# Performance work log

Hardware: AMD Instinct MI355X
Metric: run time of the kernel (lower is better)

The kernel has to match this reference:

```python
import jax, jax.numpy as jnp
import numpy as np

GRID = 16
PAD = 32
RADIUS = 8
SIGMA = 1.5
B = 8192
N_SEEDS = 24


def setup_inputs() -> dict:
    key = jax.random.key(0)
    k1, k2 = jax.random.split(key)
    # predicted seeds: (x, y, phase), coords in [0, GRID)
    output = jax.random.uniform(k1, (B, N_SEEDS * 3), dtype=jnp.float32) * GRID
    # target seeds: (x, y, amp), coords in [0, 2*GRID)
    targets = jax.random.uniform(k2, (B, N_SEEDS * 3), dtype=jnp.float32) * (2 * GRID)
    return {"output": output, "targets": targets}


def _forward(output, targets):
    Bn = output.shape[0]
    seeds = output.reshape(Bn, -1, 3)   # (B, N, 3): x, y, phase
    tgt = targets.reshape(Bn, -1, 3)    # (B, M, 3): x, y, amp

    # --- discrete Voronoi on GRID x GRID (vectorized over batch) ---
    c = jnp.arange(GRID, dtype=output.dtype)
    xx, yy = jnp.meshgrid(c, c, indexing='ij')  # (GRID, GRID)
    dist = jnp.sqrt((xx[None, :, :, None] - seeds[:, None, None, :, 0]) ** 2
                    + (yy[None, :, :, None] - seeds[:, None, None, :, 1]) ** 2)
    labels = jnp.argmin(dist, axis=-1)  # (B, GRID, GRID) int

    # circular support on the inner grid (np.ogrid[-r:r, -r:r] convention)
    cc = jnp.arange(-RADIUS, RADIUS)
    inner = (cc[:, None] ** 2 + cc[None, :] ** 2) <= RADIUS ** 2
    labels = jnp.where(inner[None], labels, 0)

    # zero-pad voronoi labels to PAD x PAD
    pw = (PAD - GRID) // 2
    padded = jnp.pad(labels, ((0, 0), (pw, pw), (pw, pw)))  # (B, PAD, PAD)

    # --- gather phase per pixel, zero outside circle on padded grid ---
    phases = seeds[:, :, 2]  # (B, N)
    phase = jnp.take_along_axis(phases, padded.reshape(Bn, -1), axis=1).reshape(Bn, PAD, PAD)
    pc = jnp.arange(PAD)
    center = PAD // 2
    outside = (pc[:, None] - center) ** 2 + (pc[None, :] - center) ** 2 > RADIUS ** 2
    phase = jnp.where(outside[None], jnp.zeros_like(phase), phase)

    # --- density = amp(=1) * exp(i * 2*pi * phase), shifted FFT magnitude ---
    two_pi = 2.0 * jnp.pi
    density = jax.lax.complex(jnp.cos(two_pi * phase), jnp.sin(two_pi * phase))
    pred = jnp.fft.fftshift(density, axes=(-2, -1))
    pred = jnp.fft.fft2(pred)
    pred_dp = jnp.abs(jnp.fft.fftshift(pred, axes=(-2, -1)))  # (B, PAD, PAD)

    # --- target diffraction: sum of Gaussians on (2*GRID)x(2*GRID) grid ---
    xc = jnp.arange(PAD, dtype=targets.dtype)  # height == width == 2*GRID == PAD
    tx = tgt[:, :, 0][:, :, None, None]
    ty = tgt[:, :, 1][:, :, None, None]
    amp = tgt[:, :, 2][:, :, None, None]
    # torch: x varies along last axis, y along second-to-last
    d2 = (xc[None, None, None, :] - tx) ** 2 + (xc[None, None, :, None] - ty) ** 2
    tgt_dp = jnp.sum(amp * jnp.exp(-d2 / (2.0 * SIGMA ** 2)), axis=1)  # (B, PAD, PAD)

    # --- chi-square (global max-normalization and reductions) ---
    p = pred_dp / jnp.max(pred_dp)
    t = tgt_dp / jnp.max(tgt_dp)
    return jnp.sum((p - t) ** 2) / jnp.sqrt(jnp.sum(p ** 2) * jnp.sum(t ** 2))


def reference(output, targets):
    return _forward(output, targets)
```

## Files before the change

### kernel.cpp

```cpp
#include <hip/hip_runtime.h>
#include <math.h>

#define NS 24


#define ROT() { float nr_ = cr*wr - ci*wi, ni_ = cr*wi + ci*wr; cr = nr_; ci = ni_; }

struct PixTab { unsigned short v[196]; };
__device__ constexpr PixTab make_pix() {
    PixTab t{};
    int n = 0;
    const int w[16] = {0,3,5,6,6,7,7,7,8,7,7,7,6,6,5,3};
    for (int yy = 0; yy < 16; ++yy)
        for (int x = 16 - w[yy]; x <= 16 + w[yy]; ++x)
            if (x < 24) { t.v[n] = (unsigned short)((yy << 8) | x); n = n + 1; }
    t.v[195] = (unsigned short)((8 << 8) | 24);
    return t;
}
__device__ constexpr PixTab PIX = make_pix();

__global__ __launch_bounds__(256)
void loss_main(const float* __restrict__ output, const float* __restrict__ targets,
               float* __restrict__ partials, int B) {
    __shared__ float2 sxy[NS];
    __shared__ float sp[NS];
    __shared__ float tx[NS], ty[NS], ta[NS];
    __shared__ float2 e24s;
    __shared__ float gx[NS * 32], gy[NS * 32];
    __shared__ float2 e2[16 * 33];
    __shared__ float gTre[32 * 20], gTim[32 * 20];
    __shared__ float pm[32 * 40];
    __shared__ float redm[4][5];

    const int b = blockIdx.x;
    const int t = threadIdx.x;
    const float* so = output + b * NS * 3;
    const float* tg = targets + b * NS * 3;

    if (t < NS) {
        sxy[t] = make_float2(so[3 * t + 0], so[3 * t + 1]);
        sp[t] = so[3 * t + 2];
        if (t == 0) {
            float sv0, cv0;
            __sincosf(6.2831853071795864f * sp[0], &sv0, &cv0);
            e24s = make_float2(cv0 - 1.0f, sv0);
        }
    }
    if (t >= 64 && t < 64 + NS) {
        int s = t - 64;
        tx[s] = tg[3 * s + 0];
        ty[s] = tg[3 * s + 1];
        ta[s] = tg[3 * s + 2];
    }
    for (int i = t; i < 16 * 33; i += 256) e2[i] = make_float2(0.0f, 0.0f);
    __syncthreads();

    for (int idx = t; idx < NS * 32; idx += 256) {
        int s = idx >> 5, c = idx & 31;
        float dx = (float)c - tx[s];
        gx[idx] = ta[s] * __expf(dx * dx * (-1.0f / 4.5f));
        float dy = (float)c - ty[s];
        gy[idx] = __expf(dy * dy * (-1.0f / 4.5f));
    }

    if (t < 196) {
        int pv = (int)PIX.v[t];
        int yy = pv >> 8, x = pv & 255;
        float ph;
        if (t < 195) {
            float fi = (float)yy, fj = (float)(x - 8);
            int best = 0;
            float bd = 1e30f;
#pragma unroll
            for (int s = 0; s < NS; ++s) {
                float2 sv = sxy[s];
                float ddx = fi - sv.x, ddy = fj - sv.y;
                float d2 = ddx * ddx + ddy * ddy;
                if (d2 < bd) { bd = d2; best = s; }
            }
            ph = sp[best];
        } else {
            ph = sp[0];
        }
        float sv_, cv_;
        __sincosf(6.2831853071795864f * ph, &sv_, &cv_);
        e2[yy * 33 + x] = make_float2(cv_ - 1.0f, sv_);
    }
    __syncthreads();

    {
        int yy = t >> 4;
        int l0 = t & 15;
        int m = l0 & 3;
        float cr = (m == 0) ? 1.f : (m == 2) ? -1.f : 0.f;
        float ci = (m == 1) ? -1.f : (m == 3) ? 1.f : 0.f;
        float wr, wi;
        __sincosf(-(float)l0 * 0.19634954084936207f, &wi, &wr);
        float g0r = 0, g0i = 0, g1r = 0, g1i = 0;
        const float2* row = &e2[yy * 33];
#pragma unroll
        for (int xp = 0; xp < 8; ++xp) {
            int x = 8 + 2 * xp;
            float2 a = row[x];
            float tr = a.x * cr - a.y * ci, ti = a.x * ci + a.y * cr;
            g0r += tr; g0i += ti; g1r += tr; g1i += ti;
            ROT();
            float2 bb = row[x + 1];
            tr = bb.x * cr - bb.y * ci; ti = bb.x * ci + bb.y * cr;
            g0r += tr; g0i += ti; g1r -= tr; g1i -= ti;
            ROT();
        }
        {
            float2 a = row[24];
            float tr = a.x * cr - a.y * ci, ti = a.x * ci + a.y * cr;
            g0r += tr; g0i += ti; g1r += tr; g1i += ti;
        }
        gTre[l0 * 20 + yy] = g0r;        gTim[l0 * 20 + yy] = g0i;
        gTre[(l0 + 16) * 20 + yy] = g1r; gTim[(l0 + 16) * 20 + yy] = g1i;
    }
    __syncthreads();

    {
        int l = t >> 3;
        int k0 = t & 7;
        int m = k0 & 3;
        float cr = (m == 0) ? 1.f : (m == 2) ? -1.f : 0.f;
        float ci = (m == 1) ? -1.f : (m == 3) ? 1.f : 0.f;
        float wr, wi;
        __sincosf(-(float)k0 * 0.19634954084936207f, &wi, &wr);
        float h0r = 0, h0i = 0, h1r = 0, h1i = 0, h2r = 0, h2i = 0, h3r = 0, h3i = 0;
#pragma unroll
        for (int c4 = 0; c4 < 4; ++c4) {
            float4 gr = *(const float4*)&gTre[l * 20 + 4 * c4];
            float4 gi = *(const float4*)&gTim[l * 20 + 4 * c4];
            float tr, ti;
            tr = gr.x * cr - gi.x * ci; ti = gr.x * ci + gi.x * cr;
            h0r += tr; h0i += ti;
            h1r += tr; h1i += ti;
            h2r += tr; h2i += ti;
            h3r += tr; h3i += ti;
            ROT();
            tr = gr.y * cr - gi.y * ci; ti = gr.y * ci + gi.y * cr;
            h0r += tr; h0i += ti;
            h1r += ti; h1i -= tr;
            h2r -= tr; h2i -= ti;
            h3r -= ti; h3i += tr;
            ROT();
            tr = gr.z * cr - gi.z * ci; ti = gr.z * ci + gi.z * cr;
            h0r += tr; h0i += ti;
            h1r -= tr; h1i -= ti;
            h2r += tr; h2i += ti;
            h3r -= tr; h3i -= ti;
            ROT();
            tr = gr.w * cr - gi.w * ci; ti = gr.w * ci + gi.w * cr;
            h0r += tr; h0i += ti;
            h1r -= ti; h1i += tr;
            h2r -= tr; h2i -= ti;
            h3r += ti; h3i -= tr;
            ROT();
        }
        {
            float2 e24 = e24s;
            float ar2 = (m == 0) ? 1.f : (m == 2) ? -1.f : 0.f;
            float ai2 = (m == 1) ? 1.f : (m == 3) ? -1.f : 0.f;
            float sgn = (l & 1) ? -1.f : 1.f;
            float Tr = sgn * (e24.x * ar2 - e24.y * ai2);
            float Ti = sgn * (e24.x * ai2 + e24.y * ar2);
            h0r += Tr; h0i += Ti;
            h1r += Tr; h1i += Ti;
            h2r += Tr; h2i += Ti;
            h3r += Tr; h3i += Ti;
        }
        if (t == 0) h0r += 1024.0f;
        int v = (l + 16) & 31;
        pm[((k0 + 16) & 31) * 40 + v] = sqrtf(h0r * h0r + h0i * h0i);
        pm[((k0 + 24) & 31) * 40 + v] = sqrtf(h1r * h1r + h1i * h1i);
        pm[(k0)        * 40 + v]      = sqrtf(h2r * h2r + h2i * h2i);
        pm[((k0 + 8))  * 40 + v]      = sqrtf(h3r * h3r + h3i * h3i);
    }
    __syncthreads();

    float mp = 0.f, mt = 0.f, sp2 = 0.f, st2 = 0.f, spt = 0.f;
    {
        int r = t >> 3;
        int c0 = (t & 7) * 4;
        float4 p4 = *(const float4*)&pm[r * 40 + c0];
        float t0 = 0, t1 = 0, t2 = 0, t3 = 0;
#pragma unroll
        for (int s = 0; s < NS; ++s) {
            float gyv = gy[s * 32 + r];
            float4 g4 = *(const float4*)&gx[s * 32 + c0];
            t0 += gyv * g4.x; t1 += gyv * g4.y;
            t2 += gyv * g4.z; t3 += gyv * g4.w;
        }
        mp = fmaxf(fmaxf(p4.x, p4.y), fmaxf(p4.z, p4.w));
        mt = fmaxf(fmaxf(t0, t1), fmaxf(t2, t3));
        sp2 = p4.x * p4.x + p4.y * p4.y + p4.z * p4.z + p4.w * p4.w;
        st2 = t0 * t0 + t1 * t1 + t2 * t2 + t3 * t3;
        spt = p4.x * t0 + p4.y * t1 + p4.z * t2 + p4.w * t3;
    }

    for (int off = 32; off > 0; off >>= 1) {
        mp  = fmaxf(mp, __shfl_down(mp, off));
        mt  = fmaxf(mt, __shfl_down(mt, off));
        sp2 += __shfl_down(sp2, off);
        st2 += __shfl_down(st2, off);
        spt += __shfl_down(spt, off);
    }
    int wave = t >> 6, lane = t & 63;
    if (lane == 0) {
        redm[wave][0] = sp2; redm[wave][1] = st2; redm[wave][2] = spt;
        redm[wave][3] = mp;  redm[wave][4] = mt;
    }
    __syncthreads();
    if (t == 0) {
        for (int w = 1; w < 4; ++w) {
            sp2 += redm[w][0];
            st2 += redm[w][1];
            spt += redm[w][2];
            mp = fmaxf(mp, redm[w][3]);
            mt = fmaxf(mt, redm[w][4]);
        }
        partials[0 * B + b] = sp2;
        partials[1 * B + b] = st2;
        partials[2 * B + b] = spt;
        partials[3 * B + b] = mp;
        partials[4 * B + b] = mt;
    }
}

__global__ __launch_bounds__(1024)
void finalize_loss(const float* __restrict__ partials, float* __restrict__ out, int B) {
    __shared__ double reds[16][3];
    __shared__ float redx[16][2];
    const int t = threadIdx.x;
    double sp2 = 0.0, st2 = 0.0, spt = 0.0;
    float mp = 0.f, mt = 0.f;
    for (int i = t; i < B; i += 1024) {
        sp2 += (double)partials[0 * B + i];
        st2 += (double)partials[1 * B + i];
        spt += (double)partials[2 * B + i];
        mp = fmaxf(mp, partials[3 * B + i]);
        mt = fmaxf(mt, partials[4 * B + i]);
    }
    for (int off = 32; off > 0; off >>= 1) {
        sp2 += __shfl_down(sp2, off);
        st2 += __shfl_down(st2, off);
        spt += __shfl_down(spt, off);
        mp = fmaxf(mp, __shfl_down(mp, off));
        mt = fmaxf(mt, __shfl_down(mt, off));
    }
    int wave = t >> 6, lane = t & 63;
    if (lane == 0) {
        reds[wave][0] = sp2; reds[wave][1] = st2; reds[wave][2] = spt;
        redx[wave][0] = mp;  redx[wave][1] = mt;
    }
    __syncthreads();
    if (t == 0) {
        for (int w = 1; w < 16; ++w) {
            sp2 += reds[w][0];
            st2 += reds[w][1];
            spt += reds[w][2];
            mp = fmaxf(mp, redx[w][0]);
            mt = fmaxf(mt, redx[w][1]);
        }
        double Mp = (double)mp, Mt = (double)mt;
        double loss = (sp2 * (Mt / Mp) + st2 * (Mp / Mt) - 2.0 * spt) / sqrt(sp2 * st2);
        out[0] = (float)loss;
    }
}

extern "C" void kernel_launch(void* const* d_in, const int* in_sizes, int n_in,
                              void* d_out, int out_size, void* d_ws, size_t ws_size,
                              hipStream_t stream) {
    const float* output  = (const float*)d_in[0];
    const float* targets = (const float*)d_in[1];
    int B = in_sizes[0] / (NS * 3);
    float* partials = (float*)d_ws;

    loss_main<<<B, 256, 0, stream>>>(output, targets, partials, B);
    finalize_loss<<<1, 1024, 0, stream>>>(partials, (float*)d_out, B);
}
```

Measured before the change: 109.6 us.

## Use precomputed shared-memory twiddle tables and packed float2 math in DFT stages

Replaces the per-thread recurrence twiddle rotations in both DFT stages with tables of exact twiddles built once per block in shared memory (aliased with the magnitude buffer). Complex multiplies and reductions are rewritten with 2-wide vector types and fma so the compiler can emit packed FP32 instructions. The gT buffer is interleaved re/im with padding so each thread reads it with vector loads. The intent is to shorten the ALU dependency chains, at the cost of extra LDS traffic and a table-building step.

```diff
diff --git a/kernel.cpp b/kernel.cpp
--- a/kernel.cpp
+++ b/kernel.cpp
@@ -3,8 +3,9 @@
 
 #define NS 24
 
-
-#define ROT() { float nr_ = cr*wr - ci*wi, ni_ = cr*wi + ci*wr; cr = nr_; ci = ni_; }
+typedef float v2f __attribute__((ext_vector_type(2)));
+typedef float v4f __attribute__((ext_vector_type(4)));
+
 
 struct PixTab { unsigned short v[196]; };
 __device__ constexpr PixTab make_pix() {
@@ -19,6 +20,10 @@
 }
 __device__ constexpr PixTab PIX = make_pix();
 
+#define CMUL(e_, w4_) \
+    __builtin_elementwise_fma((v2f){(e_).y, (e_).y}, (v2f){(w4_).z, (w4_).w}, \
+                              (v2f){(e_).x, (e_).x} * (v2f){(w4_).x, (w4_).y})
+
 __global__ __launch_bounds__(256)
 void loss_main(const float* __restrict__ output, const float* __restrict__ targets,
                float* __restrict__ partials, int B) {
@@ -26,11 +31,15 @@
     __shared__ float sp[NS];
     __shared__ float tx[NS], ty[NS], ta[NS];
     __shared__ float2 e24s;
-    __shared__ float gx[NS * 32], gy[NS * 32];
-    __shared__ float2 e2[16 * 33];
-    __shared__ float gTre[32 * 20], gTim[32 * 20];
-    __shared__ float pm[32 * 40];
+    __shared__ __align__(16) float gx[NS * 32], gy[NS * 32];
+    __shared__ __align__(16) float e2f[16 * 33 * 2];
+    __shared__ __align__(16) float tw2f[16 * 8 * 4];
+    __shared__ __align__(16) float gT2f[32 * 36];
+    __shared__ __align__(16) char uA[5120];
     __shared__ float redm[4][5];
+
+    float* tw1f = (float*)uA;
+    float* pmf  = (float*)uA;
 
     const int b = blockIdx.x;
     const int t = threadIdx.x;
@@ -52,7 +61,7 @@
         ty[s] = tg[3 * s + 1];
         ta[s] = tg[3 * s + 2];
     }
-    for (int i = t; i < 16 * 33; i += 256) e2[i] = make_float2(0.0f, 0.0f);
+    for (int i = t; i < 16 * 33; i += 256) *(v2f*)&e2f[i * 2] = (v2f){0.f, 0.f};
     __syncthreads();
 
     for (int idx = t; idx < NS * 32; idx += 256) {
@@ -61,6 +70,24 @@
         gx[idx] = ta[s] * __expf(dx * dx * (-1.0f / 4.5f));
         float dy = (float)c - ty[s];
         gy[idx] = __expf(dy * dy * (-1.0f / 4.5f));
+    }
+
+    for (int i = t; i < 400; i += 256) {
+        int p;
+        float* dst;
+        if (i < 272) {
+            int xp = i >> 4, l0 = i & 15;
+            p = (l0 * (xp + 8)) & 31;
+            dst = &tw1f[i * 4];
+        } else {
+            int j = i - 272;
+            int yp = j >> 3, k0 = j & 7;
+            p = (k0 * (yp + 8)) & 31;
+            dst = &tw2f[j * 4];
+        }
+        float si, co;
+        __sincosf(-(float)p * 0.19634954084936207f, &si, &co);
+        dst[0] = co; dst[1] = si; dst[2] = -si; dst[3] = co;
     }
 
     if (t < 196) {
@@ -84,120 +111,104 @@
         }
         float sv_, cv_;
         __sincosf(6.2831853071795864f * ph, &sv_, &cv_);
-        e2[yy * 33 + x] = make_float2(cv_ - 1.0f, sv_);
+        *(v2f*)&e2f[(yy * 33 + x) * 2] = (v2f){cv_ - 1.0f, sv_};
     }
     __syncthreads();
 
     {
-        int yy = t >> 4;
-        int l0 = t & 15;
-        int m = l0 & 3;
-        float cr = (m == 0) ? 1.f : (m == 2) ? -1.f : 0.f;
-        float ci = (m == 1) ? -1.f : (m == 3) ? 1.f : 0.f;
-        float wr, wi;
-        __sincosf(-(float)l0 * 0.19634954084936207f, &wi, &wr);
-        float g0r = 0, g0i = 0, g1r = 0, g1i = 0;
-        const float2* row = &e2[yy * 33];
-#pragma unroll
-        for (int xp = 0; xp < 8; ++xp) {
-            int x = 8 + 2 * xp;
-            float2 a = row[x];
-            float tr = a.x * cr - a.y * ci, ti = a.x * ci + a.y * cr;
-            g0r += tr; g0i += ti; g1r += tr; g1i += ti;
-            ROT();
-            float2 bb = row[x + 1];
-            tr = bb.x * cr - bb.y * ci; ti = bb.x * ci + bb.y * cr;
-            g0r += tr; g0i += ti; g1r -= tr; g1i -= ti;
-            ROT();
-        }
-        {
-            float2 a = row[24];
-            float tr = a.x * cr - a.y * ci, ti = a.x * ci + a.y * cr;
-            g0r += tr; g0i += ti; g1r += tr; g1i += ti;
-        }
-        gTre[l0 * 20 + yy] = g0r;        gTim[l0 * 20 + yy] = g0i;
-        gTre[(l0 + 16) * 20 + yy] = g1r; gTim[(l0 + 16) * 20 + yy] = g1i;
+        int yy = t >> 4, l0 = t & 15;
+        v2f g0 = {0.f, 0.f}, g1 = {0.f, 0.f};
+        const int rb = (yy * 33 + 8) * 2;
+#pragma unroll
+        for (int xp = 0; xp < 17; ++xp) {
+            v2f e = *(const v2f*)&e2f[rb + xp * 2];
+            v4f w4 = *(const v4f*)&tw1f[(xp * 16 + l0) * 4];
+            v2f tt = CMUL(e, w4);
+            g0 += tt;
+            if (xp & 1) g1 -= tt; else g1 += tt;
+        }
+        *(v2f*)&gT2f[l0 * 36 + yy * 2] = g0;
+        *(v2f*)&gT2f[(l0 + 16) * 36 + yy * 2] = g1;
     }
     __syncthreads();
 
     {
-        int l = t >> 3;
-        int k0 = t & 7;
-        int m = k0 & 3;
-        float cr = (m == 0) ? 1.f : (m == 2) ? -1.f : 0.f;
-        float ci = (m == 1) ? -1.f : (m == 3) ? 1.f : 0.f;
-        float wr, wi;
-        __sincosf(-(float)k0 * 0.19634954084936207f, &wi, &wr);
-        float h0r = 0, h0i = 0, h1r = 0, h1i = 0, h2r = 0, h2i = 0, h3r = 0, h3i = 0;
-#pragma unroll
-        for (int c4 = 0; c4 < 4; ++c4) {
-            float4 gr = *(const float4*)&gTre[l * 20 + 4 * c4];
-            float4 gi = *(const float4*)&gTim[l * 20 + 4 * c4];
-            float tr, ti;
-            tr = gr.x * cr - gi.x * ci; ti = gr.x * ci + gi.x * cr;
-            h0r += tr; h0i += ti;
-            h1r += tr; h1i += ti;
-            h2r += tr; h2i += ti;
-            h3r += tr; h3i += ti;
-            ROT();
-            tr = gr.y * cr - gi.y * ci; ti = gr.y * ci + gi.y * cr;
-            h0r += tr; h0i += ti;
-            h1r += ti; h1i -= tr;
-            h2r -= tr; h2i -= ti;
-            h3r -= ti; h3i += tr;
-            ROT();
-            tr = gr.z * cr - gi.z * ci; ti = gr.z * ci + gi.z * cr;
-            h0r += tr; h0i += ti;
-            h1r -= tr; h1i -= ti;
-            h2r += tr; h2i += ti;
-            h3r -= tr; h3i -= ti;
-            ROT();
-            tr = gr.w * cr - gi.w * ci; ti = gr.w * ci + gi.w * cr;
-            h0r += tr; h0i += ti;
-            h1r -= ti; h1i += tr;
-            h2r -= tr; h2i -= ti;
-            h3r += ti; h3i -= tr;
-            ROT();
+        int l = t >> 3, k0 = t & 7;
+        v2f h0 = {0,0}, h1 = {0,0}, h2 = {0,0}, h3 = {0,0};
+#pragma unroll
+        for (int q = 0; q < 4; ++q) {
+            v4f ga = *(const v4f*)&gT2f[l * 36 + q * 8];
+            v4f gb = *(const v4f*)&gT2f[l * 36 + q * 8 + 4];
+            {
+                v4f w4 = *(const v4f*)&tw2f[((4 * q) * 8 + k0) * 4];
+                v2f ge = {ga.x, ga.y};
+                v2f tt = CMUL(ge, w4);
+                h0 += tt; h1 += tt; h2 += tt; h3 += tt;
+            }
+            {
+                v4f w4 = *(const v4f*)&tw2f[((4 * q + 1) * 8 + k0) * 4];
+                v2f ge = {ga.z, ga.w};
+                v2f tt = CMUL(ge, w4);
+                v2f u = {tt.y, -tt.x};
+                h0 += tt; h1 += u; h2 -= tt; h3 -= u;
+            }
+            {
+                v4f w4 = *(const v4f*)&tw2f[((4 * q + 2) * 8 + k0) * 4];
+                v2f ge = {gb.x, gb.y};
+                v2f tt = CMUL(ge, w4);
+                h0 += tt; h1 -= tt; h2 += tt; h3 -= tt;
+            }
+            {
+                v4f w4 = *(const v4f*)&tw2f[((4 * q + 3) * 8 + k0) * 4];
+                v2f ge = {gb.z, gb.w};
+                v2f tt = CMUL(ge, w4);
+                v2f u = {tt.y, -tt.x};
+                h0 += tt; h1 -= u; h2 -= tt; h3 += u;
+            }
         }
         {
             float2 e24 = e24s;
+            int m = k0 & 3;
             float ar2 = (m == 0) ? 1.f : (m == 2) ? -1.f : 0.f;
             float ai2 = (m == 1) ? 1.f : (m == 3) ? -1.f : 0.f;
             float sgn = (l & 1) ? -1.f : 1.f;
-            float Tr = sgn * (e24.x * ar2 - e24.y * ai2);
-            float Ti = sgn * (e24.x * ai2 + e24.y * ar2);
-            h0r += Tr; h0i += Ti;
-            h1r += Tr; h1i += Ti;
-            h2r += Tr; h2i += Ti;
-            h3r += Tr; h3i += Ti;
-        }
-        if (t == 0) h0r += 1024.0f;
+            v2f T = {sgn * (e24.x * ar2 - e24.y * ai2),
+                     sgn * (e24.x * ai2 + e24.y * ar2)};
+            h0 += T; h1 += T; h2 += T; h3 += T;
+        }
+        if (t == 0) h0.x += 1024.0f;
         int v = (l + 16) & 31;
-        pm[((k0 + 16) & 31) * 40 + v] = sqrtf(h0r * h0r + h0i * h0i);
-        pm[((k0 + 24) & 31) * 40 + v] = sqrtf(h1r * h1r + h1i * h1i);
-        pm[(k0)        * 40 + v]      = sqrtf(h2r * h2r + h2i * h2i);
-        pm[((k0 + 8))  * 40 + v]      = sqrtf(h3r * h3r + h3i * h3i);
-    }
-    __syncthreads();
-
-    float mp = 0.f, mt = 0.f, sp2 = 0.f, st2 = 0.f, spt = 0.f;
+        v2f q0 = h0 * h0, q1 = h1 * h1, q2 = h2 * h2, q3 = h3 * h3;
+        pmf[((k0 + 16) & 31) * 40 + v] = sqrtf(q0.x + q0.y);
+        pmf[((k0 + 24) & 31) * 40 + v] = sqrtf(q1.x + q1.y);
+        pmf[(k0)        * 40 + v]      = sqrtf(q2.x + q2.y);
+        pmf[(k0 + 8)    * 40 + v]      = sqrtf(q3.x + q3.y);
+    }
+    __syncthreads();
+
+    float mp, mt, sp2, st2, spt;
     {
         int r = t >> 3;
         int c0 = (t & 7) * 4;
-        float4 p4 = *(const float4*)&pm[r * 40 + c0];
-        float t0 = 0, t1 = 0, t2 = 0, t3 = 0;
+        v4f p4 = *(const v4f*)&pmf[r * 40 + c0];
+        v2f t01 = {0.f, 0.f}, t23 = {0.f, 0.f};
 #pragma unroll
         for (int s = 0; s < NS; ++s) {
             float gyv = gy[s * 32 + r];
-            float4 g4 = *(const float4*)&gx[s * 32 + c0];
-            t0 += gyv * g4.x; t1 += gyv * g4.y;
-            t2 += gyv * g4.z; t3 += gyv * g4.w;
-        }
+            v4f g4 = *(const v4f*)&gx[s * 32 + c0];
+            v2f gv = {gyv, gyv};
+            t01 = __builtin_elementwise_fma(gv, (v2f){g4.x, g4.y}, t01);
+            t23 = __builtin_elementwise_fma(gv, (v2f){g4.z, g4.w}, t23);
+        }
+        v2f p01 = {p4.x, p4.y}, p23 = {p4.z, p4.w};
+        v2f s2v = __builtin_elementwise_fma(p23, p23, p01 * p01);
+        v2f t2v = __builtin_elementwise_fma(t23, t23, t01 * t01);
+        v2f ptv = __builtin_elementwise_fma(p23, t23, p01 * t01);
+        sp2 = s2v.x + s2v.y;
+        st2 = t2v.x + t2v.y;
+        spt = ptv.x + ptv.y;
         mp = fmaxf(fmaxf(p4.x, p4.y), fmaxf(p4.z, p4.w));
-        mt = fmaxf(fmaxf(t0, t1), fmaxf(t2, t3));
-        sp2 = p4.x * p4.x + p4.y * p4.y + p4.z * p4.z + p4.w * p4.w;
-        st2 = t0 * t0 + t1 * t1 + t2 * t2 + t3 * t3;
-        spt = p4.x * t0 + p4.y * t1 + p4.z * t2 + p4.w * t3;
+        mt = fmaxf(fmaxf(t01.x, t01.y), fmaxf(t23.x, t23.y));
     }
 
     for (int off = 32; off > 0; off >>= 1) {
```

Measured after the change: 107.9 us. About the same (-1.5%).
